# Optimization experiments

Hardware: AMD Instinct MI355X
Metric: run time of the kernel (lower is better)

## Reference

```python
import jax, jax.numpy as jnp
import numpy as np

B, N, F_IN = 512, 128, 133
NHID, NHEADS, HID = 64, 8, 512
FP_DIM, FP2, TASKS = 1489, 512, 12
ALPHA = 0.2
NEG_BIG = -9e15


def _lin_init(key, fan_in, fan_out):
    return jax.random.normal(key, (fan_in, fan_out), jnp.float32) / np.sqrt(fan_in)


def setup_inputs() -> dict:
    key = jax.random.key(0)
    ks = jax.random.split(key, 24)
    inp = {
        'h': jax.random.normal(ks[0], (B, N, F_IN), jnp.float32),
        'adj': jax.random.randint(ks[1], (B, N, N), 0, 2, jnp.int32),
        'edge_feat': jax.random.uniform(ks[2], (B, N, N), jnp.float32),
        'fp': jax.random.uniform(ks[3], (B, FP_DIM), jnp.float32),
        # multi-head GAT layer params (a split as [a1; a2; a_edge])
        'W_heads': jax.random.normal(ks[4], (NHEADS, F_IN, NHID), jnp.float32) / np.sqrt(F_IN),
        'a1_heads': jax.random.normal(ks[5], (NHEADS, NHID), jnp.float32) / np.sqrt(NHID),
        'a2_heads': jax.random.normal(ks[6], (NHEADS, NHID), jnp.float32) / np.sqrt(NHID),
        'ae_heads': jax.random.normal(ks[7], (NHEADS,), jnp.float32) * 0.1,
        # output GAT layer
        'W_out': jax.random.normal(ks[8], (NHID * NHEADS, HID), jnp.float32) / np.sqrt(NHID * NHEADS),
        'a1_out': jax.random.normal(ks[9], (HID,), jnp.float32) / np.sqrt(HID),
        'a2_out': jax.random.normal(ks[10], (HID,), jnp.float32) / np.sqrt(HID),
        'ae_out': jax.random.normal(ks[11], ()) * 0.1,
        # FPN
        'fc1_w': _lin_init(ks[12], FP_DIM, FP2), 'fc1_b': jnp.zeros((FP2,), jnp.float32),
        'fc2_w': _lin_init(ks[13], FP2, HID), 'fc2_b': jnp.zeros((HID,), jnp.float32),
        # cross-attention fusion
        'q_w': _lin_init(ks[14], HID, HID), 'q_b': jnp.zeros((HID,), jnp.float32),
        'k_w': _lin_init(ks[15], HID, HID), 'k_b': jnp.zeros((HID,), jnp.float32),
        'v_w': _lin_init(ks[16], HID, HID), 'v_b': jnp.zeros((HID,), jnp.float32),
        'o_w': _lin_init(ks[17], HID, HID), 'o_b': jnp.zeros((HID,), jnp.float32),
        # FFN head
        'ffn1_w': _lin_init(ks[18], HID, HID), 'ffn1_b': jnp.zeros((HID,), jnp.float32),
        'ffn2_w': _lin_init(ks[19], HID, TASKS), 'ffn2_b': jnp.zeros((TASKS,), jnp.float32),
    }
    return inp


def _leaky(x):
    return jnp.where(x >= 0, x, ALPHA * x)


def _fpgnn_forward(h, adj, edge_feat, fp,
                   W_heads, a1_heads, a2_heads, ae_heads,
                   W_out, a1_out, a2_out, ae_out,
                   fc1_w, fc1_b, fc2_w, fc2_b,
                   q_w, q_b, k_w, k_b, v_w, v_b, o_w, o_b,
                   ffn1_w, ffn1_b, ffn2_w, ffn2_b):
    mask = adj > 0  # [B,N,N]
    # --- multi-head GAT layers (concat=True) ---
    Wh = jnp.einsum('bnf,hfd->bhnd', h, W_heads)            # [B,H,N,D]
    s1 = jnp.einsum('bhnd,hd->bhn', Wh, a1_heads)
    s2 = jnp.einsum('bhnd,hd->bhn', Wh, a2_heads)
    # e[b,h,i,j] = leaky(Wh_i.a1 + Wh_j.a2 + edge_ij*ae)  (exact decomposition of
    # the original concat([Wh_i, Wh_j, edge_ij]) @ a)
    e = _leaky(s1[:, :, :, None] + s2[:, :, None, :]
               + edge_feat[:, None, :, :] * ae_heads[None, :, None, None])
    att = jnp.where(mask[:, None], e, NEG_BIG)
    att = jax.nn.softmax(att, axis=-1)                       # softmax over dim=1 of [N,N]
    hp = jnp.einsum('bhij,bhjd->bhid', att, Wh)
    x = jax.nn.elu(hp)                                       # concat=True -> ELU
    x = jnp.transpose(x, (0, 2, 1, 3)).reshape(B, N, NHEADS * NHID)
    # --- output GAT layer (concat=False) ---
    Wx = x @ W_out                                           # [B,N,HID]
    t1 = Wx @ a1_out                                         # [B,N]
    t2 = Wx @ a2_out
    e2 = _leaky(t1[:, :, None] + t2[:, None, :] + edge_feat * ae_out)
    att2 = jnp.where(mask, e2, NEG_BIG)
    att2 = jax.nn.softmax(att2, axis=-1)
    hp2 = jnp.einsum('bij,bjd->bid', att2, Wx)
    gat_nodes = jax.nn.elu(hp2)                              # F.elu in GATOne
    gat_out = gat_nodes.mean(axis=1)                         # molecule readout [B,HID]
    # --- FPN ---
    fpn_out = jax.nn.relu(fp @ fc1_w + fc1_b) @ fc2_w + fc2_b  # [B,HID]
    # --- cross-attention fusion ---
    q = gat_out @ q_w + q_b
    k = fpn_out @ k_w + k_b
    v = fpn_out @ v_w + v_b
    score = jnp.sum(q * k, axis=-1, keepdims=True) / np.sqrt(HID)  # [B,1]
    weight = jax.nn.softmax(score[:, :, None], axis=-1)[:, :, 0]    # softmax over size-1 dim -> ones
    fused = q + weight * v
    fused = jax.nn.relu(fused @ o_w + o_b)
    # --- FFN head (dropout p=0, eval) ---
    out = jax.nn.relu(fused @ ffn1_w + ffn1_b) @ ffn2_w + ffn2_b
    return out


def reference(h, adj, edge_feat, fp,
              W_heads, a1_heads, a2_heads, ae_heads,
              W_out, a1_out, a2_out, ae_out,
              fc1_w, fc1_b, fc2_w, fc2_b,
              q_w, q_b, k_w, k_b, v_w, v_b, o_w, o_b,
              ffn1_w, ffn1_b, ffn2_w, ffn2_b):
    return _fpgnn_forward(h, adj, edge_feat, fp,
                          W_heads, a1_heads, a2_heads, ae_heads,
                          W_out, a1_out, a2_out, ae_out,
                          fc1_w, fc1_b, fc2_w, fc2_b,
                          q_w, q_b, k_w, k_b, v_w, v_b, o_w, o_b,
                          ffn1_w, ffn1_b, ffn2_w, ffn2_b)
```

## Files before the change

kernel.cpp:

```cpp
#include <hip/hip_runtime.h>
#include <hip/hip_bf16.h>


#define ALPHA_LK 0.2f
#define KP1 192
#define KPF 1536
#define MINF_BF16 0xFF80u

typedef unsigned short ushort_t;
typedef __attribute__((ext_vector_type(8))) short bfrag;
typedef __attribute__((ext_vector_type(4))) float ffrag;

__device__ __forceinline__ float b2f(ushort_t u) {
  return __uint_as_float(((unsigned)u) << 16);
}
__device__ __forceinline__ ushort_t f2b(float f) {
  unsigned u = __float_as_uint(f);
  unsigned r = (u + 0x7fffu + ((u >> 16) & 1u)) >> 16;
  return (ushort_t)r;
}
__device__ __forceinline__ float elu1(float v) {
  return v > 0.f ? v : __expf(v) - 1.f;
}
__device__ __forceinline__ void unpack8(uint4 u, ushort_t* e) {
  e[0] = u.x & 0xffff; e[1] = u.x >> 16;
  e[2] = u.y & 0xffff; e[3] = u.y >> 16;
  e[4] = u.z & 0xffff; e[5] = u.z >> 16;
  e[6] = u.w & 0xffff; e[7] = u.w >> 16;
}
__device__ __forceinline__ uint4 pack8(const ushort_t* o) {
  uint4 u;
  u.x = o[0] | ((unsigned)o[1] << 16);
  u.y = o[2] | ((unsigned)o[3] << 16);
  u.z = o[4] | ((unsigned)o[5] << 16);
  u.w = o[6] | ((unsigned)o[7] << 16);
  return u;
}

__global__ __launch_bounds__(256) void repack_h(const float* __restrict__ h,
                                                ushort_t* __restrict__ hb) {
  int o = blockIdx.x * 256 + threadIdx.x;
  int row = o / 48, c4 = (o - row * 48) * 4;
  const float* hr = h + (size_t)row * 133;
  ushort4 v;
  v.x = (c4 + 0 < 133) ? f2b(hr[c4 + 0]) : (ushort_t)0;
  v.y = (c4 + 1 < 133) ? f2b(hr[c4 + 1]) : (ushort_t)0;
  v.z = (c4 + 2 < 133) ? f2b(hr[c4 + 2]) : (ushort_t)0;
  v.w = (c4 + 3 < 133) ? f2b(hr[c4 + 3]) : (ushort_t)0;
  *(ushort4*)&hb[(size_t)row * KP1 + c4] = v;
}

__global__ __launch_bounds__(256) void repack_fp(const float* __restrict__ fp,
                                                 ushort_t* __restrict__ fpb) {
  int o = blockIdx.x * 256 + threadIdx.x;
  int row = o / 384, c4 = (o - row * 384) * 4;
  const float* fr = fp + (size_t)row * 1489;
  ushort4 v;
  v.x = (c4 + 0 < 1489) ? f2b(fr[c4 + 0]) : (ushort_t)0;
  v.y = (c4 + 1 < 1489) ? f2b(fr[c4 + 1]) : (ushort_t)0;
  v.z = (c4 + 2 < 1489) ? f2b(fr[c4 + 2]) : (ushort_t)0;
  v.w = (c4 + 3 < 1489) ? f2b(fr[c4 + 3]) : (ushort_t)0;
  *(ushort4*)&fpb[(size_t)row * KPF + c4] = v;
}

__global__ __launch_bounds__(256) void repack_w2t(const float* __restrict__ Whd,
                                                  ushort_t* __restrict__ W2t) {
  int o = blockIdx.x * 256 + threadIdx.x;
  if (o >= 512 * 48) return;
  int col = o / 48, c4 = (o - col * 48) * 4;
  int hh = col >> 6, d = col & 63;
  ushort4 v;
  v.x = (c4 + 0 < 133) ? f2b(Whd[(hh * 133 + c4 + 0) * 64 + d]) : (ushort_t)0;
  v.y = (c4 + 1 < 133) ? f2b(Whd[(hh * 133 + c4 + 1) * 64 + d]) : (ushort_t)0;
  v.z = (c4 + 2 < 133) ? f2b(Whd[(hh * 133 + c4 + 2) * 64 + d]) : (ushort_t)0;
  v.w = (c4 + 3 < 133) ? f2b(Whd[(hh * 133 + c4 + 3) * 64 + d]) : (ushort_t)0;
  *(ushort4*)&W2t[(size_t)col * KP1 + c4] = v;
}

__global__ __launch_bounds__(256) void repack_t(const float* __restrict__ W,
                                                ushort_t* __restrict__ Wt,
                                                int K, int N, int Kpad) {
  int kp4 = Kpad >> 2;
  int o = blockIdx.x * 256 + threadIdx.x;
  if (o >= N * kp4) return;
  int col = o / kp4, k4 = (o - col * kp4) * 4;
  ushort4 v;
  v.x = (k4 + 0 < K) ? f2b(W[(size_t)(k4 + 0) * N + col]) : (ushort_t)0;
  v.y = (k4 + 1 < K) ? f2b(W[(size_t)(k4 + 1) * N + col]) : (ushort_t)0;
  v.z = (k4 + 2 < K) ? f2b(W[(size_t)(k4 + 2) * N + col]) : (ushort_t)0;
  v.w = (k4 + 3 < K) ? f2b(W[(size_t)(k4 + 3) * N + col]) : (ushort_t)0;
  *(ushort4*)&Wt[(size_t)col * Kpad + k4] = v;
}

__global__ __launch_bounds__(256) void repack_t7(
    const float* __restrict__ w0, const float* __restrict__ w1,
    const float* __restrict__ w2, const float* __restrict__ w3,
    const float* __restrict__ w4, const float* __restrict__ w5,
    const float* __restrict__ qb, const float* __restrict__ vb,
    ushort_t* __restrict__ d0, ushort_t* __restrict__ d1,
    ushort_t* __restrict__ d2, ushort_t* __restrict__ d3,
    ushort_t* __restrict__ d4, ushort_t* __restrict__ d5,
    float* __restrict__ qvb) {
  int y = blockIdx.y;
  int o = blockIdx.x * 256 + threadIdx.x;
  if (y == 6) {
    if (o < 512) qvb[o] = qb[o] + vb[o];
    return;
  }
  const float* W = y == 0 ? w0 : y == 1 ? w1 : y == 2 ? w2
                 : y == 3 ? w3 : y == 4 ? w4 : w5;
  ushort_t* Wt = y == 0 ? d0 : y == 1 ? d1 : y == 2 ? d2
               : y == 3 ? d3 : y == 4 ? d4 : d5;
  int col = o >> 7, k4 = (o & 127) * 4;
  ushort4 v;
  v.x = f2b(W[(size_t)(k4 + 0) * 512 + col]);
  v.y = f2b(W[(size_t)(k4 + 1) * 512 + col]);
  v.z = f2b(W[(size_t)(k4 + 2) * 512 + col]);
  v.w = f2b(W[(size_t)(k4 + 3) * 512 + col]);
  *(ushort4*)&Wt[(size_t)col * 512 + k4] = v;
}

__global__ __launch_bounds__(256) void repack_em(const float* __restrict__ edge,
                                                 const int* __restrict__ adj,
                                                 ushort_t* __restrict__ em) {
  size_t o = ((size_t)blockIdx.x * 256 + threadIdx.x) * 4;
  float4 e = *(const float4*)&edge[o];
  int4 a = *(const int4*)&adj[o];
  ushort4 v;
  v.x = a.x > 0 ? f2b(e.x) : (ushort_t)MINF_BF16;
  v.y = a.y > 0 ? f2b(e.y) : (ushort_t)MINF_BF16;
  v.z = a.z > 0 ? f2b(e.z) : (ushort_t)MINF_BF16;
  v.w = a.w > 0 ? f2b(e.w) : (ushort_t)MINF_BF16;
  *(ushort4*)&em[o] = v;
}

__global__ __launch_bounds__(256) void wa12_kernel(
    const float* __restrict__ W, const float* __restrict__ a1,
    const float* __restrict__ a2, float* __restrict__ wa1,
    float* __restrict__ wa2) {
  int wv = threadIdx.x >> 6, lane = threadIdx.x & 63;
  int k = blockIdx.x * 4 + wv;
  const float* wr = W + (size_t)k * 512;
  float p1 = 0.f, p2 = 0.f;
#pragma unroll
  for (int i = 0; i < 8; ++i) {
    float v = wr[lane + i * 64];
    p1 += v * a1[lane + i * 64];
    p2 += v * a2[lane + i * 64];
  }
#pragma unroll
  for (int off = 32; off; off >>= 1) {
    p1 += __shfl_down(p1, off);
    p2 += __shfl_down(p2, off);
  }
  if (lane == 0) { wa1[k] = p1; wa2[k] = p2; }
}

__global__ __launch_bounds__(256) void t12x_kernel(
    const ushort_t* __restrict__ xb, const float* __restrict__ wa1,
    const float* __restrict__ wa2, float* __restrict__ t1o,
    float* __restrict__ t2o, int base) {
  int wv = threadIdx.x >> 6, lane = threadIdx.x & 63;
  int row = blockIdx.x * 4 + wv;
  const ushort_t* xr = xb + (size_t)row * 512;
  ushort4 u0 = *(const ushort4*)&xr[lane * 8];
  ushort4 u1 = *(const ushort4*)&xr[lane * 8 + 4];
  float xv[8] = {b2f(u0.x), b2f(u0.y), b2f(u0.z), b2f(u0.w),
                 b2f(u1.x), b2f(u1.y), b2f(u1.z), b2f(u1.w)};
  float p1 = 0.f, p2 = 0.f;
#pragma unroll
  for (int i = 0; i < 8; ++i) {
    p1 += xv[i] * wa1[lane * 8 + i];
    p2 += xv[i] * wa2[lane * 8 + i];
  }
#pragma unroll
  for (int off = 32; off; off >>= 1) {
    p1 += __shfl_down(p1, off);
    p2 += __shfl_down(p2, off);
  }
  if (lane == 0) {
    t1o[base * 128 + row] = p1;
    t2o[base * 128 + row] = p2;
  }
}

__global__ __launch_bounds__(256) void fused_gat1(
    const ushort_t* __restrict__ hb, const ushort_t* __restrict__ W2t,
    const ushort_t* __restrict__ edgeM, const float* __restrict__ a1h,
    const float* __restrict__ a2h, const float* __restrict__ ae,
    ushort_t* __restrict__ x, int base) {
  __shared__ union {
    struct { ushort_t As[128][72]; ushort_t Bs[64][72]; } g;
    ushort_t WS[64][136];
  } u;
  __shared__ float ss1[128], ss2[128];
  const int id = blockIdx.x;
  const int hh = (id >> 3) & 7;
  const int bl = ((id >> 6) << 3) | (id & 7);
  const int bg = base + bl;
  const int t = threadIdx.x;
  const int lane = t & 63, w = t >> 6;
  const int l16 = lane & 15, quad = lane >> 4;
  const int sr = t >> 3, sc = (t & 7) * 8;

  ffrag acc[2][4];
#pragma unroll
  for (int mi = 0; mi < 2; ++mi)
#pragma unroll
    for (int ni = 0; ni < 4; ++ni) acc[mi][ni] = {0.f, 0.f, 0.f, 0.f};
  for (int k0 = 0; k0 < KP1; k0 += 64) {
    __syncthreads();
#pragma unroll
    for (int p = 0; p < 4; ++p) {
      int r = p * 32 + sr;
      *(uint4*)&u.g.As[r][sc] =
          *(const uint4*)&hb[(size_t)(bl * 128 + r) * KP1 + k0 + sc];
    }
#pragma unroll
    for (int p = 0; p < 2; ++p) {
      int r = p * 32 + sr;
      *(uint4*)&u.g.Bs[r][sc] =
          *(const uint4*)&W2t[(size_t)(hh * 64 + r) * KP1 + k0 + sc];
    }
    __syncthreads();
#pragma unroll
    for (int ks = 0; ks < 2; ++ks) {
      bfrag af[2], bf[4];
#pragma unroll
      for (int mi = 0; mi < 2; ++mi)
        af[mi] = *(const bfrag*)&u.g.As[w * 32 + mi * 16 + l16][ks * 32 + quad * 8];
#pragma unroll
      for (int ni = 0; ni < 4; ++ni)
        bf[ni] = *(const bfrag*)&u.g.Bs[ni * 16 + l16][ks * 32 + quad * 8];
#pragma unroll
      for (int mi = 0; mi < 2; ++mi)
#pragma unroll
        for (int ni = 0; ni < 4; ++ni)
          acc[mi][ni] = __builtin_amdgcn_mfma_f32_16x16x32_bf16(
              af[mi], bf[ni], acc[mi][ni], 0, 0, 0);
    }
  }
  __syncthreads();

#pragma unroll
  for (int mi = 0; mi < 2; ++mi)
#pragma unroll
    for (int ni = 0; ni < 4; ++ni) {
      int col = ni * 16 + l16;
      int rowb = w * 32 + mi * 16 + quad * 4;
      ushort4 v;
      v.x = f2b(acc[mi][ni][0]);
      v.y = f2b(acc[mi][ni][1]);
      v.z = f2b(acc[mi][ni][2]);
      v.w = f2b(acc[mi][ni][3]);
      *(ushort4*)&u.WS[col][rowb] = v;
    }
  __syncthreads();

  uint4 ereg[2][4];
  {
    const ushort_t* em = edgeM + (size_t)bg * 16384;
#pragma unroll
    for (int mi = 0; mi < 2; ++mi) {
      int row = w * 32 + mi * 16 + l16;
#pragma unroll
      for (int ks = 0; ks < 4; ++ks)
        ereg[mi][ks] = *(const uint4*)&em[row * 128 + ks * 32 + quad * 8];
    }
  }
  {
    int n = t & 127;
    const float* av = (t < 128) ? a1h : a2h;
    float p = 0.f;
#pragma unroll 8
    for (int d = 0; d < 64; ++d) p += b2f(u.WS[d][n]) * av[hh * 64 + d];
    if (t < 128) ss1[n] = p; else ss2[n] = p;
  }
  __syncthreads();

  const float aeh = ae[hh];
  float rs1[2];
  rs1[0] = ss1[w * 32 + l16];
  rs1[1] = ss1[w * 32 + 16 + l16];
  uint4 aw[2][4];
  float rsum[2];
#pragma unroll
  for (int mi = 0; mi < 2; ++mi) {
    rsum[mi] = 0.f;
#pragma unroll
    for (int ks = 0; ks < 4; ++ks) {
      ushort_t eu[8], ou[8];
      unpack8(ereg[mi][ks], eu);
#pragma unroll
      for (int k = 0; k < 8; ++k) {
        float e = rs1[mi] + ss2[ks * 32 + quad * 8 + k] + b2f(eu[k]) * aeh;
        e = e >= 0.f ? e : ALPHA_LK * e;
        float pexp = (eu[k] != MINF_BF16) ? __expf(e) : 0.f;
        ou[k] = f2b(pexp);
        rsum[mi] += b2f(ou[k]);
      }
      aw[mi][ks] = pack8(ou);
    }
    rsum[mi] += __shfl_xor(rsum[mi], 16);
    rsum[mi] += __shfl_xor(rsum[mi], 32);
  }
  float sinv0 = 1.f / fmaxf(rsum[0], 1e-30f);
  float sinv1 = 1.f / fmaxf(rsum[1], 1e-30f);

  ffrag acc2[2][4];
#pragma unroll
  for (int mi = 0; mi < 2; ++mi)
#pragma unroll
    for (int ni = 0; ni < 4; ++ni) acc2[mi][ni] = {0.f, 0.f, 0.f, 0.f};
#pragma unroll
  for (int ks = 0; ks < 4; ++ks) {
    bfrag bfr[4];
#pragma unroll
    for (int ni = 0; ni < 4; ++ni)
      bfr[ni] = *(const bfrag*)&u.WS[ni * 16 + l16][ks * 32 + quad * 8];
#pragma unroll
    for (int mi = 0; mi < 2; ++mi) {
      bfrag afr;
      __builtin_memcpy(&afr, &aw[mi][ks], 16);
#pragma unroll
      for (int ni = 0; ni < 4; ++ni)
        acc2[mi][ni] = __builtin_amdgcn_mfma_f32_16x16x32_bf16(
            afr, bfr[ni], acc2[mi][ni], 0, 0, 0);
    }
  }
  float sv[2][4];
#pragma unroll
  for (int r = 0; r < 4; ++r) {
    sv[0][r] = __shfl(sinv0, quad * 4 + r);
    sv[1][r] = __shfl(sinv1, quad * 4 + r);
  }
#pragma unroll
  for (int mi = 0; mi < 2; ++mi)
#pragma unroll
    for (int ni = 0; ni < 4; ++ni)
#pragma unroll
      for (int r = 0; r < 4; ++r) {
        int rl = w * 32 + mi * 16 + quad * 4 + r;
        x[(size_t)(bl * 128 + rl) * 512 + hh * 64 + ni * 16 + l16] =
            f2b(elu1(acc2[mi][ni][r] * sv[mi][r]));
      }
}

__global__ __launch_bounds__(256) void fused_gat2(
    const ushort_t* __restrict__ xb, const ushort_t* __restrict__ Wot,
    const ushort_t* __restrict__ edgeM, const float* __restrict__ t1,
    const float* __restrict__ t2, const float* __restrict__ aeo,
    ushort_t* __restrict__ gatb, int base) {
  __shared__ union {
    struct { ushort_t As[128][72]; ushort_t Bs[128][72]; } g;
    ushort_t WS[128][136];
  } u;
  __shared__ float st1[128], st2[128];
  __shared__ float ps[4][64];
  const int id = blockIdx.x;
  const int sp2 = (id >> 3) & 3;
  const int bl = ((id >> 5) << 3) | (id & 7);
  const int bg = base + bl;
  const int t = threadIdx.x;
  const int lane = t & 63, w = t >> 6;
  const int wm = w >> 1, wn = w & 1;
  const int l16 = lane & 15, quad = lane >> 4;
  const int sr = t >> 3, sc = (t & 7) * 8;

  if (t < 128) {
    st1[t] = t1[bg * 128 + t];
    st2[t] = t2[bg * 128 + t];
  }

  ffrag acc[4][4];
#pragma unroll
  for (int mi = 0; mi < 4; ++mi)
#pragma unroll
    for (int ni = 0; ni < 4; ++ni) acc[mi][ni] = {0.f, 0.f, 0.f, 0.f};
  for (int k0 = 0; k0 < 512; k0 += 64) {
    __syncthreads();
#pragma unroll
    for (int p = 0; p < 4; ++p) {
      int r = p * 32 + sr;
      *(uint4*)&u.g.As[r][sc] =
          *(const uint4*)&xb[(size_t)(bl * 128 + r) * 512 + k0 + sc];
      *(uint4*)&u.g.Bs[r][sc] =
          *(const uint4*)&Wot[(size_t)(sp2 * 128 + r) * 512 + k0 + sc];
    }
    __syncthreads();
#pragma unroll
    for (int ks = 0; ks < 2; ++ks) {
      bfrag af[4], bf[4];
#pragma unroll
      for (int i = 0; i < 4; ++i) {
        af[i] = *(const bfrag*)&u.g.As[wm * 64 + i * 16 + l16][ks * 32 + quad * 8];
        bf[i] = *(const bfrag*)&u.g.Bs[wn * 64 + i * 16 + l16][ks * 32 + quad * 8];
      }
#pragma unroll
      for (int mi = 0; mi < 4; ++mi)
#pragma unroll
        for (int ni = 0; ni < 4; ++ni)
          acc[mi][ni] = __builtin_amdgcn_mfma_f32_16x16x32_bf16(
              af[mi], bf[ni], acc[mi][ni], 0, 0, 0);
    }
  }
  __syncthreads();

#pragma unroll
  for (int mi = 0; mi < 4; ++mi)
#pragma unroll
    for (int ni = 0; ni < 4; ++ni) {
      int col = wn * 64 + ni * 16 + l16;
      int rowb = wm * 64 + mi * 16 + quad * 4;
      ushort4 v;
      v.x = f2b(acc[mi][ni][0]);
      v.y = f2b(acc[mi][ni][1]);
      v.z = f2b(acc[mi][ni][2]);
      v.w = f2b(acc[mi][ni][3]);
      *(ushort4*)&u.WS[col][rowb] = v;
    }
  __syncthreads();

  const float ae = aeo[0];
  uint4 aw[2][4];
  float rsum[2];
  {
    const ushort_t* em = edgeM + (size_t)bg * 16384;
#pragma unroll
    for (int mi = 0; mi < 2; ++mi) {
      int row = w * 32 + mi * 16 + l16;
      float rs1 = st1[row];
      rsum[mi] = 0.f;
#pragma unroll
      for (int ks = 0; ks < 4; ++ks) {
        ushort_t eu[8], ou[8];
        unpack8(*(const uint4*)&em[row * 128 + ks * 32 + quad * 8], eu);
#pragma unroll
        for (int k = 0; k < 8; ++k) {
          float e = rs1 + st2[ks * 32 + quad * 8 + k] + b2f(eu[k]) * ae;
          e = e >= 0.f ? e : ALPHA_LK * e;
          float pexp = (eu[k] != MINF_BF16) ? __expf(e) : 0.f;
          ou[k] = f2b(pexp);
          rsum[mi] += b2f(ou[k]);
        }
        aw[mi][ks] = pack8(ou);
      }
      rsum[mi] += __shfl_xor(rsum[mi], 16);
      rsum[mi] += __shfl_xor(rsum[mi], 32);
    }
  }
  float sinv0 = 1.f / fmaxf(rsum[0], 1e-30f);
  float sinv1 = 1.f / fmaxf(rsum[1], 1e-30f);
  float sv[2][4];
#pragma unroll
  for (int r = 0; r < 4; ++r) {
    sv[0][r] = __shfl(sinv0, quad * 4 + r);
    sv[1][r] = __shfl(sinv1, quad * 4 + r);
  }

  for (int s0 = 0; s0 < 2; ++s0) {
    ffrag acc2[2][4];
#pragma unroll
    for (int mi = 0; mi < 2; ++mi)
#pragma unroll
      for (int ni = 0; ni < 4; ++ni) acc2[mi][ni] = {0.f, 0.f, 0.f, 0.f};
#pragma unroll
    for (int ks = 0; ks < 4; ++ks) {
      bfrag bfr[4];
#pragma unroll
      for (int ni = 0; ni < 4; ++ni)
        bfr[ni] = *(const bfrag*)&u.WS[s0 * 64 + ni * 16 + l16][ks * 32 + quad * 8];
#pragma unroll
      for (int mi = 0; mi < 2; ++mi) {
        bfrag afr;
        __builtin_memcpy(&afr, &aw[mi][ks], 16);
#pragma unroll
        for (int ni = 0; ni < 4; ++ni)
          acc2[mi][ni] = __builtin_amdgcn_mfma_f32_16x16x32_bf16(
              afr, bfr[ni], acc2[mi][ni], 0, 0, 0);
      }
    }
    __syncthreads();
#pragma unroll
    for (int ni = 0; ni < 4; ++ni) {
      float s = 0.f;
#pragma unroll
      for (int mi = 0; mi < 2; ++mi)
#pragma unroll
        for (int r = 0; r < 4; ++r) s += elu1(acc2[mi][ni][r] * sv[mi][r]);
      s += __shfl_xor(s, 16);
      s += __shfl_xor(s, 32);
      if (quad == 0) ps[w][ni * 16 + l16] = s;
    }
    __syncthreads();
    if (t < 64) {
      float s = ps[0][t] + ps[1][t] + ps[2][t] + ps[3][t];
      gatb[(size_t)bg * 512 + sp2 * 128 + s0 * 64 + t] = f2b(s * (1.f / 128.f));
    }
  }
}

__device__ __forceinline__ void tail_kloop(
    const ushort_t* __restrict__ A, const ushort_t* __restrict__ Bt,
    int K, int ld, ushort_t (*As)[72], ushort_t (*Bs)[72],
    ffrag (*acc)[4], int row0, int col0, int t) {
  const int lane = t & 63, w = t >> 6;
  const int wm = w >> 1, wn = w & 1;
  const int l16 = lane & 15, quad = lane >> 4;
  const int sr = t >> 3, sc = (t & 7) * 8;
  for (int k0 = 0; k0 < K; k0 += 64) {
    __syncthreads();
#pragma unroll
    for (int p = 0; p < 4; ++p) {
      int r = p * 32 + sr;
      *(uint4*)&As[r][sc] = *(const uint4*)&A[(size_t)(row0 + r) * ld + k0 + sc];
      *(uint4*)&Bs[r][sc] = *(const uint4*)&Bt[(size_t)(col0 + r) * ld + k0 + sc];
    }
    __syncthreads();
#pragma unroll
    for (int ks = 0; ks < 2; ++ks) {
      bfrag af[4], bf[4];
#pragma unroll
      for (int i = 0; i < 4; ++i) {
        af[i] = *(const bfrag*)&As[wm * 64 + i * 16 + l16][ks * 32 + quad * 8];
        bf[i] = *(const bfrag*)&Bs[wn * 64 + i * 16 + l16][ks * 32 + quad * 8];
      }
#pragma unroll
      for (int mi = 0; mi < 4; ++mi)
#pragma unroll
        for (int ni = 0; ni < 4; ++ni)
          acc[mi][ni] = __builtin_amdgcn_mfma_f32_16x16x32_bf16(
              af[mi], bf[ni], acc[mi][ni], 0, 0, 0);
    }
  }
}

template <int DUAL, int RELU>
__global__ __launch_bounds__(256) void gemm_tail(
    const ushort_t* __restrict__ A1, const ushort_t* __restrict__ Bt1,
    int K1, int ld1,
    const ushort_t* __restrict__ A2, const ushort_t* __restrict__ Bt2,
    const float* __restrict__ bias, ushort_t* __restrict__ C) {
  __shared__ ushort_t As[128][72];
  __shared__ ushort_t Bs[128][72];
  const int t = threadIdx.x;
  const int lane = t & 63, w = t >> 6;
  const int wm = w >> 1, wn = w & 1;
  const int l16 = lane & 15, quad = lane >> 4;
  const int row0 = blockIdx.y * 128, col0 = blockIdx.x * 128;

  ffrag acc[4][4];
#pragma unroll
  for (int mi = 0; mi < 4; ++mi)
#pragma unroll
    for (int ni = 0; ni < 4; ++ni) acc[mi][ni] = {0.f, 0.f, 0.f, 0.f};

  tail_kloop(A1, Bt1, K1, ld1, As, Bs, acc, row0, col0, t);
  if (DUAL) tail_kloop(A2, Bt2, 512, 512, As, Bs, acc, row0, col0, t);

#pragma unroll
  for (int mi = 0; mi < 4; ++mi)
#pragma unroll
    for (int ni = 0; ni < 4; ++ni) {
      int col = col0 + wn * 64 + ni * 16 + l16;
      float bb = bias[col];
#pragma unroll
      for (int r = 0; r < 4; ++r) {
        int row = row0 + wm * 64 + mi * 16 + quad * 4 + r;
        float v = acc[mi][ni][r] + bb;
        if (RELU) v = fmaxf(v, 0.f);
        C[(size_t)row * 512 + col] = f2b(v);
      }
    }
}

__global__ __launch_bounds__(256) void ffn2_kernel(
    const ushort_t* __restrict__ f5, const float* __restrict__ W,
    const float* __restrict__ b, float* __restrict__ out) {
  int wv = threadIdx.x >> 6, lane = threadIdx.x & 63;
  int row = blockIdx.x * 4 + wv;
  const ushort_t* fr = f5 + (size_t)row * 512;
  float v[8];
  ushort4 u0 = *(const ushort4*)&fr[lane * 8];
  ushort4 u1 = *(const ushort4*)&fr[lane * 8 + 4];
  v[0] = b2f(u0.x); v[1] = b2f(u0.y); v[2] = b2f(u0.z); v[3] = b2f(u0.w);
  v[4] = b2f(u1.x); v[5] = b2f(u1.y); v[6] = b2f(u1.z); v[7] = b2f(u1.w);
#pragma unroll
  for (int j = 0; j < 12; ++j) {
    float s = 0.f;
#pragma unroll
    for (int i = 0; i < 8; ++i) s += v[i] * W[(size_t)(lane * 8 + i) * 12 + j];
#pragma unroll
    for (int off = 32; off; off >>= 1) s += __shfl_down(s, off);
    if (lane == 0) out[(size_t)row * 12 + j] = s + b[j];
  }
}

extern "C" void kernel_launch(void* const* d_in, const int* in_sizes, int n_in,
                              void* d_out, int out_size, void* d_ws, size_t ws_size,
                              hipStream_t stream) {
  const float* h        = (const float*)d_in[0];
  const int*   adj      = (const int*)d_in[1];
  const float* edge     = (const float*)d_in[2];
  const float* fp       = (const float*)d_in[3];
  const float* W_heads  = (const float*)d_in[4];
  const float* a1_heads = (const float*)d_in[5];
  const float* a2_heads = (const float*)d_in[6];
  const float* ae_heads = (const float*)d_in[7];
  const float* W_out  = (const float*)d_in[8];
  const float* a1_out = (const float*)d_in[9];
  const float* a2_out = (const float*)d_in[10];
  const float* ae_out = (const float*)d_in[11];
  const float* fc1_w = (const float*)d_in[12];
  const float* fc1_b = (const float*)d_in[13];
  const float* fc2_w = (const float*)d_in[14];
  const float* fc2_b = (const float*)d_in[15];
  const float* q_w = (const float*)d_in[16];
  const float* q_b = (const float*)d_in[17];
  const float* v_w = (const float*)d_in[20];
  const float* v_b = (const float*)d_in[21];
  const float* o_w = (const float*)d_in[22];
  const float* o_b = (const float*)d_in[23];
  const float* ffn1_w = (const float*)d_in[24];
  const float* ffn1_b = (const float*)d_in[25];
  const float* ffn2_w = (const float*)d_in[26];
  const float* ffn2_b = (const float*)d_in[27];
  float* out = (float*)d_out;

  const size_t hb_bytes = (size_t)65536 * KP1 * 2;
  const size_t em_bytes = (size_t)512 * 16384 * 2;
  const size_t tail_bytes =
      (size_t)512 * KPF * 2 * 2 + (size_t)512 * 512 * 2 * 12 + 2048;
  const size_t fixed_bytes = hb_bytes + em_bytes + (size_t)512 * KP1 * 2 +
                             (size_t)2 * 65536 * 4 + tail_bytes + 16384;
  int C = 32;
  for (int cand = 512; cand >= 32; cand >>= 1) {
    size_t need = (size_t)cand * 131072 + fixed_bytes;
    if (need <= ws_size) { C = cand; break; }
  }
  const int M = C * 128;

  char* p = (char*)d_ws;
  ushort_t* xb  = (ushort_t*)p; p += (size_t)C * 65536 * 2;
  ushort_t* hb  = (ushort_t*)p; p += hb_bytes;
  ushort_t* em  = (ushort_t*)p; p += em_bytes;
  ushort_t* W2t = (ushort_t*)p; p += (size_t)512 * KP1 * 2;
  float* t1 = (float*)p; p += 65536 * 4;
  float* t2 = (float*)p; p += 65536 * 4;
  ushort_t* fpb  = (ushort_t*)p; p += (size_t)512 * KPF * 2;
  ushort_t* fc1t = (ushort_t*)p; p += (size_t)512 * KPF * 2;
  ushort_t* Wot  = (ushort_t*)p; p += (size_t)512 * 512 * 2;
  ushort_t* fc2t = (ushort_t*)p; p += (size_t)512 * 512 * 2;
  ushort_t* qwt  = (ushort_t*)p; p += (size_t)512 * 512 * 2;
  ushort_t* vwt  = (ushort_t*)p; p += (size_t)512 * 512 * 2;
  ushort_t* owt  = (ushort_t*)p; p += (size_t)512 * 512 * 2;
  ushort_t* f1t  = (ushort_t*)p; p += (size_t)512 * 512 * 2;
  ushort_t* gatb = (ushort_t*)p; p += (size_t)512 * 512 * 2;
  ushort_t* fb1  = (ushort_t*)p; p += (size_t)512 * 512 * 2;
  ushort_t* fb2  = (ushort_t*)p; p += (size_t)512 * 512 * 2;
  ushort_t* fb3  = (ushort_t*)p; p += (size_t)512 * 512 * 2;
  ushort_t* fb4  = (ushort_t*)p; p += (size_t)512 * 512 * 2;
  ushort_t* fb5  = (ushort_t*)p; p += (size_t)512 * 512 * 2;
  float* qvb = (float*)p; p += 2048;
  float* wa1 = (float*)p; p += 2048;
  float* wa2 = (float*)p; p += 2048;

  repack_h<<<12288, 256, 0, stream>>>(h, hb);
  repack_em<<<8192, 256, 0, stream>>>(edge, adj, em);
  repack_w2t<<<96, 256, 0, stream>>>(W_heads, W2t);
  repack_fp<<<768, 256, 0, stream>>>(fp, fpb);
  repack_t<<<768, 256, 0, stream>>>(fc1_w, fc1t, 1489, 512, KPF);
  repack_t7<<<dim3(256, 7), 256, 0, stream>>>(
      W_out, fc2_w, q_w, v_w, o_w, ffn1_w, q_b, v_b,
      Wot, fc2t, qwt, vwt, owt, f1t, qvb);
  wa12_kernel<<<128, 256, 0, stream>>>(W_out, a1_out, a2_out, wa1, wa2);

  for (int base = 0; base < 512; base += C) {
    fused_gat1<<<8 * C, 256, 0, stream>>>(
        hb + (size_t)base * 128 * KP1, W2t, em, a1_heads, a2_heads,
        ae_heads, xb, base);
    t12x_kernel<<<M / 4, 256, 0, stream>>>(xb, wa1, wa2, t1, t2, base);
    fused_gat2<<<4 * C, 256, 0, stream>>>(
        xb, Wot, em, t1, t2, ae_out, gatb, base);
  }

  gemm_tail<0, 1><<<dim3(4, 4), 256, 0, stream>>>(
      fpb, fc1t, KPF, KPF, nullptr, nullptr, fc1_b, fb1);
  gemm_tail<0, 0><<<dim3(4, 4), 256, 0, stream>>>(
      fb1, fc2t, 512, 512, nullptr, nullptr, fc2_b, fb2);
  gemm_tail<1, 0><<<dim3(4, 4), 256, 0, stream>>>(
      gatb, qwt, 512, 512, fb2, vwt, qvb, fb3);
  gemm_tail<0, 1><<<dim3(4, 4), 256, 0, stream>>>(
      fb3, owt, 512, 512, nullptr, nullptr, o_b, fb4);
  gemm_tail<0, 1><<<dim3(4, 4), 256, 0, stream>>>(
      fb4, f1t, 512, 512, nullptr, nullptr, ffn1_b, fb5);
  ffn2_kernel<<<128, 256, 0, stream>>>(fb5, ffn2_w, ffn2_b, out);
}
```

Before: 461.1 us.

## Use direct global-to-LDS loads with XOR swizzle and precompute layer-2 attention once

```diff
diff --git a/kernel.cpp b/kernel.cpp
--- a/kernel.cpp
+++ b/kernel.cpp
@@ -35,6 +35,13 @@
   u.z = o[4] | ((unsigned)o[5] << 16);
   u.w = o[6] | ((unsigned)o[7] << 16);
   return u;
+}
+
+__device__ __forceinline__ void gll16(const void* g, void* l) {
+  __builtin_amdgcn_global_load_lds(
+      (const __attribute__((address_space(1))) unsigned int*)(unsigned long long)g,
+      (__attribute__((address_space(3))) unsigned int*)(unsigned long long)l,
+      16, 0, 0);
 }
 
 __global__ __launch_bounds__(256) void repack_h(const float* __restrict__ h,
@@ -184,13 +191,46 @@
   }
 }
 
+__global__ __launch_bounds__(256) void att2_kernel(
+    const ushort_t* __restrict__ em, const float* __restrict__ t1,
+    const float* __restrict__ t2, const float* __restrict__ aeo,
+    ushort_t* __restrict__ awg, float* __restrict__ sinvg, int base) {
+  __shared__ float t2s[128];
+  const int bl = blockIdx.x, bg = base + bl;
+  const int t = threadIdx.x;
+  if (t < 128) t2s[t] = t2[(size_t)bg * 128 + t];
+  __syncthreads();
+  const int row = t >> 1, half = t & 1;
+  const float ae = aeo[0];
+  const float rt1 = t1[(size_t)bg * 128 + row];
+  const ushort_t* emr = em + (size_t)bg * 16384 + row * 128 + half * 64;
+  ushort_t* awr = awg + (size_t)bl * 16384 + row * 128 + half * 64;
+  float s = 0.f;
+#pragma unroll
+  for (int v = 0; v < 8; ++v) {
+    ushort_t eu[8], ou[8];
+    unpack8(*(const uint4*)&emr[v * 8], eu);
+#pragma unroll
+    for (int k = 0; k < 8; ++k) {
+      float e = rt1 + t2s[half * 64 + v * 8 + k] + b2f(eu[k]) * ae;
+      e = e >= 0.f ? e : ALPHA_LK * e;
+      float pexp = (eu[k] != MINF_BF16) ? __expf(e) : 0.f;
+      ou[k] = f2b(pexp);
+      s += b2f(ou[k]);
+    }
+    *(uint4*)&awr[v * 8] = pack8(ou);
+  }
+  s += __shfl_xor(s, 1);
+  if (!half) sinvg[(size_t)bl * 128 + row] = 1.f / fmaxf(s, 1e-30f);
+}
+
 __global__ __launch_bounds__(256) void fused_gat1(
     const ushort_t* __restrict__ hb, const ushort_t* __restrict__ W2t,
     const ushort_t* __restrict__ edgeM, const float* __restrict__ a1h,
     const float* __restrict__ a2h, const float* __restrict__ ae,
     ushort_t* __restrict__ x, int base) {
   __shared__ union {
-    struct { ushort_t As[128][72]; ushort_t Bs[64][72]; } g;
+    struct { ushort_t As[128][64]; ushort_t Bs[64][64]; } g;
     ushort_t WS[64][136];
   } u;
   __shared__ float ss1[128], ss2[128];
@@ -201,8 +241,11 @@
   const int t = threadIdx.x;
   const int lane = t & 63, w = t >> 6;
   const int l16 = lane & 15, quad = lane >> 4;
-  const int sr = t >> 3, sc = (t & 7) * 8;
-
+  const int w8 = w * 8, sr8 = (t >> 3) & 7;
+  const int csw = ((t & 7) ^ sr8) << 3;
+
+  const ushort_t* gA = hb + (size_t)(bl * 128 + w8 + sr8) * KP1 + csw;
+  const ushort_t* gB = W2t + (size_t)(hh * 64 + w8 + sr8) * KP1 + csw;
   ffrag acc[2][4];
 #pragma unroll
   for (int mi = 0; mi < 2; ++mi)
@@ -211,27 +254,22 @@
   for (int k0 = 0; k0 < KP1; k0 += 64) {
     __syncthreads();
 #pragma unroll
-    for (int p = 0; p < 4; ++p) {
-      int r = p * 32 + sr;
-      *(uint4*)&u.g.As[r][sc] =
-          *(const uint4*)&hb[(size_t)(bl * 128 + r) * KP1 + k0 + sc];
-    }
-#pragma unroll
-    for (int p = 0; p < 2; ++p) {
-      int r = p * 32 + sr;
-      *(uint4*)&u.g.Bs[r][sc] =
-          *(const uint4*)&W2t[(size_t)(hh * 64 + r) * KP1 + k0 + sc];
-    }
+    for (int p = 0; p < 4; ++p)
+      gll16(gA + (size_t)(p * 32) * KP1 + k0, &u.g.As[p * 32 + w8][0]);
+#pragma unroll
+    for (int p = 0; p < 2; ++p)
+      gll16(gB + (size_t)(p * 32) * KP1 + k0, &u.g.Bs[p * 32 + w8][0]);
     __syncthreads();
 #pragma unroll
     for (int ks = 0; ks < 2; ++ks) {
+      const int cs = ((ks * 4 + quad) ^ (l16 & 7)) << 3;
       bfrag af[2], bf[4];
 #pragma unroll
       for (int mi = 0; mi < 2; ++mi)
-        af[mi] = *(const bfrag*)&u.g.As[w * 32 + mi * 16 + l16][ks * 32 + quad * 8];
+        af[mi] = *(const bfrag*)&u.g.As[w * 32 + mi * 16 + l16][cs];
 #pragma unroll
       for (int ni = 0; ni < 4; ++ni)
-        bf[ni] = *(const bfrag*)&u.g.Bs[ni * 16 + l16][ks * 32 + quad * 8];
+        bf[ni] = *(const bfrag*)&u.g.Bs[ni * 16 + l16][cs];
 #pragma unroll
       for (int mi = 0; mi < 2; ++mi)
 #pragma unroll
@@ -348,14 +386,12 @@
 
 __global__ __launch_bounds__(256) void fused_gat2(
     const ushort_t* __restrict__ xb, const ushort_t* __restrict__ Wot,
-    const ushort_t* __restrict__ edgeM, const float* __restrict__ t1,
-    const float* __restrict__ t2, const float* __restrict__ aeo,
+    const ushort_t* __restrict__ awg, const float* __restrict__ sinvg,
     ushort_t* __restrict__ gatb, int base) {
   __shared__ union {
-    struct { ushort_t As[128][72]; ushort_t Bs[128][72]; } g;
+    struct { ushort_t As[128][64]; ushort_t Bs[128][64]; } g;
     ushort_t WS[128][136];
   } u;
-  __shared__ float st1[128], st2[128];
   __shared__ float ps[4][64];
   const int id = blockIdx.x;
   const int sp2 = (id >> 3) & 3;
@@ -365,13 +401,11 @@
   const int lane = t & 63, w = t >> 6;
   const int wm = w >> 1, wn = w & 1;
   const int l16 = lane & 15, quad = lane >> 4;
-  const int sr = t >> 3, sc = (t & 7) * 8;
-
-  if (t < 128) {
-    st1[t] = t1[bg * 128 + t];
-    st2[t] = t2[bg * 128 + t];
-  }
-
+  const int w8 = w * 8, sr8 = (t >> 3) & 7;
+  const int csw = ((t & 7) ^ sr8) << 3;
+
+  const ushort_t* gA = xb + (size_t)(bl * 128 + w8 + sr8) * 512 + csw;
+  const ushort_t* gB = Wot + (size_t)(sp2 * 128 + w8 + sr8) * 512 + csw;
   ffrag acc[4][4];
 #pragma unroll
   for (int mi = 0; mi < 4; ++mi)
@@ -381,20 +415,18 @@
     __syncthreads();
 #pragma unroll
     for (int p = 0; p < 4; ++p) {
-      int r = p * 32 + sr;
-      *(uint4*)&u.g.As[r][sc] =
-          *(const uint4*)&xb[(size_t)(bl * 128 + r) * 512 + k0 + sc];
-      *(uint4*)&u.g.Bs[r][sc] =
-          *(const uint4*)&Wot[(size_t)(sp2 * 128 + r) * 512 + k0 + sc];
+      gll16(gA + (size_t)(p * 32) * 512 + k0, &u.g.As[p * 32 + w8][0]);
+      gll16(gB + (size_t)(p * 32) * 512 + k0, &u.g.Bs[p * 32 + w8][0]);
     }
     __syncthreads();
 #pragma unroll
     for (int ks = 0; ks < 2; ++ks) {
+      const int cs = ((ks * 4 + quad) ^ (l16 & 7)) << 3;
       bfrag af[4], bf[4];
 #pragma unroll
       for (int i = 0; i < 4; ++i) {
-        af[i] = *(const bfrag*)&u.g.As[wm * 64 + i * 16 + l16][ks * 32 + quad * 8];
-        bf[i] = *(const bfrag*)&u.g.Bs[wn * 64 + i * 16 + l16][ks * 32 + quad * 8];
+        af[i] = *(const bfrag*)&u.g.As[wm * 64 + i * 16 + l16][cs];
+        bf[i] = *(const bfrag*)&u.g.Bs[wn * 64 + i * 16 + l16][cs];
       }
 #pragma unroll
       for (int mi = 0; mi < 4; ++mi)
@@ -421,41 +453,20 @@
     }
   __syncthreads();
 
-  const float ae = aeo[0];
-  uint4 aw[2][4];
-  float rsum[2];
+  uint4 awf[2][4];
+  float sv[2][4];
   {
-    const ushort_t* em = edgeM + (size_t)bg * 16384;
+    const ushort_t* ap = awg + (size_t)bl * 16384;
 #pragma unroll
     for (int mi = 0; mi < 2; ++mi) {
       int row = w * 32 + mi * 16 + l16;
-      float rs1 = st1[row];
-      rsum[mi] = 0.f;
-#pragma unroll
-      for (int ks = 0; ks < 4; ++ks) {
-        ushort_t eu[8], ou[8];
-        unpack8(*(const uint4*)&em[row * 128 + ks * 32 + quad * 8], eu);
-#pragma unroll
-        for (int k = 0; k < 8; ++k) {
-          float e = rs1 + st2[ks * 32 + quad * 8 + k] + b2f(eu[k]) * ae;
-          e = e >= 0.f ? e : ALPHA_LK * e;
-          float pexp = (eu[k] != MINF_BF16) ? __expf(e) : 0.f;
-          ou[k] = f2b(pexp);
-          rsum[mi] += b2f(ou[k]);
-        }
-        aw[mi][ks] = pack8(ou);
-      }
-      rsum[mi] += __shfl_xor(rsum[mi], 16);
-      rsum[mi] += __shfl_xor(rsum[mi], 32);
-    }
-  }
-  float sinv0 = 1.f / fmaxf(rsum[0], 1e-30f);
-  float sinv1 = 1.f / fmaxf(rsum[1], 1e-30f);
-  float sv[2][4];
-#pragma unroll
-  for (int r = 0; r < 4; ++r) {
-    sv[0][r] = __shfl(sinv0, quad * 4 + r);
-    sv[1][r] = __shfl(sinv1, quad * 4 + r);
+#pragma unroll
+      for (int ks = 0; ks < 4; ++ks)
+        awf[mi][ks] = *(const uint4*)&ap[row * 128 + ks * 32 + quad * 8];
+      float si = sinvg[(size_t)bl * 128 + row];
+#pragma unroll
+      for (int r = 0; r < 4; ++r) sv[mi][r] = __shfl(si, quad * 4 + r);
+    }
   }
 
   for (int s0 = 0; s0 < 2; ++s0) {
@@ -473,7 +484,7 @@
 #pragma unroll
       for (int mi = 0; mi < 2; ++mi) {
         bfrag afr;
-        __builtin_memcpy(&afr, &aw[mi][ks], 16);
+        __builtin_memcpy(&afr, &awf[mi][ks], 16);
 #pragma unroll
         for (int ni = 0; ni < 4; ++ni)
           acc2[mi][ni] = __builtin_amdgcn_mfma_f32_16x16x32_bf16(
@@ -502,28 +513,31 @@
 
 __device__ __forceinline__ void tail_kloop(
     const ushort_t* __restrict__ A, const ushort_t* __restrict__ Bt,
-    int K, int ld, ushort_t (*As)[72], ushort_t (*Bs)[72],
+    int K, int ld, ushort_t (*As)[64], ushort_t (*Bs)[64],
     ffrag (*acc)[4], int row0, int col0, int t) {
   const int lane = t & 63, w = t >> 6;
   const int wm = w >> 1, wn = w & 1;
   const int l16 = lane & 15, quad = lane >> 4;
-  const int sr = t >> 3, sc = (t & 7) * 8;
+  const int w8 = w * 8, sr8 = (t >> 3) & 7;
+  const int csw = ((t & 7) ^ sr8) << 3;
+  const ushort_t* gA = A + (size_t)(row0 + w8 + sr8) * ld + csw;
+  const ushort_t* gB = Bt + (size_t)(col0 + w8 + sr8) * ld + csw;
   for (int k0 = 0; k0 < K; k0 += 64) {
     __syncthreads();
 #pragma unroll
     for (int p = 0; p < 4; ++p) {
-      int r = p * 32 + sr;
-      *(uint4*)&As[r][sc] = *(const uint4*)&A[(size_t)(row0 + r) * ld + k0 + sc];
-      *(uint4*)&Bs[r][sc] = *(const uint4*)&Bt[(size_t)(col0 + r) * ld + k0 + sc];
+      gll16(gA + (size_t)(p * 32) * ld + k0, &As[p * 32 + w8][0]);
+      gll16(gB + (size_t)(p * 32) * ld + k0, &Bs[p * 32 + w8][0]);
     }
     __syncthreads();
 #pragma unroll
     for (int ks = 0; ks < 2; ++ks) {
+      const int cs = ((ks * 4 + quad) ^ (l16 & 7)) << 3;
       bfrag af[4], bf[4];
 #pragma unroll
       for (int i = 0; i < 4; ++i) {
-        af[i] = *(const bfrag*)&As[wm * 64 + i * 16 + l16][ks * 32 + quad * 8];
-        bf[i] = *(const bfrag*)&Bs[wn * 64 + i * 16 + l16][ks * 32 + quad * 8];
+        af[i] = *(const bfrag*)&As[wm * 64 + i * 16 + l16][cs];
+        bf[i] = *(const bfrag*)&Bs[wn * 64 + i * 16 + l16][cs];
       }
 #pragma unroll
       for (int mi = 0; mi < 4; ++mi)
@@ -541,8 +555,8 @@
     int K1, int ld1,
     const ushort_t* __restrict__ A2, const ushort_t* __restrict__ Bt2,
     const float* __restrict__ bias, ushort_t* __restrict__ C) {
-  __shared__ ushort_t As[128][72];
-  __shared__ ushort_t Bs[128][72];
+  __shared__ ushort_t As[128][64];
+  __shared__ ushort_t Bs[128][64];
   const int t = threadIdx.x;
   const int lane = t & 63, w = t >> 6;
   const int wm = w >> 1, wn = w & 1;
@@ -635,13 +649,15 @@
                              (size_t)2 * 65536 * 4 + tail_bytes + 16384;
   int C = 32;
   for (int cand = 512; cand >= 32; cand >>= 1) {
-    size_t need = (size_t)cand * 131072 + fixed_bytes;
+    size_t need = (size_t)cand * (131072 + 32768 + 512) + fixed_bytes;
     if (need <= ws_size) { C = cand; break; }
   }
   const int M = C * 128;
 
   char* p = (char*)d_ws;
   ushort_t* xb  = (ushort_t*)p; p += (size_t)C * 65536 * 2;
+  ushort_t* awg = (ushort_t*)p; p += (size_t)C * 16384 * 2;
+  float* sinv   = (float*)p;    p += (size_t)C * 128 * 4;
   ushort_t* hb  = (ushort_t*)p; p += hb_bytes;
   ushort_t* em  = (ushort_t*)p; p += em_bytes;
   ushort_t* W2t = (ushort_t*)p; p += (size_t)512 * KP1 * 2;
@@ -680,8 +696,8 @@
         hb + (size_t)base * 128 * KP1, W2t, em, a1_heads, a2_heads,
         ae_heads, xb, base);
     t12x_kernel<<<M / 4, 256, 0, stream>>>(xb, wa1, wa2, t1, t2, base);
-    fused_gat2<<<4 * C, 256, 0, stream>>>(
-        xb, Wot, em, t1, t2, ae_out, gatb, base);
+    att2_kernel<<<C, 256, 0, stream>>>(em, t1, t2, ae_out, awg, sinv, base);
+    fused_gat2<<<4 * C, 256, 0, stream>>>(xb, Wot, awg, sinv, gatb, base);
   }
 
   gemm_tail<0, 1><<<dim3(4, 4), 256, 0, stream>>>(
```

Result: no change. 460.3 us (-0.2%).
